# Kernel tuning notes

Measured on AMD Instinct MI355X. Metric: run time of the kernel, lower is better.

## Reference

```python
import jax, jax.numpy as jnp
import numpy as np

B, S, HID = 2, 2048, 2048
NH, NKV, HD = 16, 8, 128
GATE = NH  # headwise gate logits
KV_DIM = NKV * HD
QKV_OUT = NH * HD + GATE + 2 * KV_DIM  # 4112


def rotate_half(x):
    x1, x2 = jnp.split(x, 2, axis=-1)
    return jnp.concatenate([-x2, x1], axis=-1)


def setup_inputs() -> dict:
    key = jax.random.key(0)
    k1, k2, k3, k4, k5 = jax.random.split(key, 5)
    return {
        "hidden_states": jax.random.normal(k1, (B, S, HID), dtype=jnp.float32),
        "cos": jax.random.uniform(k2, (S, HD), dtype=jnp.float32),
        "sin": jax.random.uniform(k3, (S, HD), dtype=jnp.float32),
        "w_qkv": jax.random.normal(k4, (QKV_OUT, HID), dtype=jnp.float32) * (1.0 / HID ** 0.5),
        "w_o": jax.random.normal(k5, (HID, NH * HD), dtype=jnp.float32) * (1.0 / (NH * HD) ** 0.5),
    }


def reference(hidden_states, cos, sin, w_qkv, w_o):
    b, s, _ = hidden_states.shape
    qkv = hidden_states @ w_qkv.T  # [B,S,4112]
    q = qkv[..., :HID].reshape(b, s, NH, HD)
    gate = qkv[..., HID:HID + GATE]  # [B,S,NH]
    k = qkv[..., HID + GATE:HID + GATE + KV_DIM].reshape(b, s, NKV, HD)
    v = qkv[..., HID + GATE + KV_DIM:].reshape(b, s, NKV, HD)
    # RoPE (cos/sin broadcast over batch and heads)
    c = cos[None, :, None, :]
    sn = sin[None, :, None, :]
    q = q * c + rotate_half(q) * sn
    k = k * c + rotate_half(k) * sn
    # GQA: repeat kv heads (repeat_interleave on head axis)
    rep = NH // NKV
    k = jnp.repeat(k, rep, axis=2)
    v = jnp.repeat(v, rep, axis=2)
    scores = jnp.einsum("bqhd,bkhd->bhqk", q, k) / jnp.sqrt(jnp.float32(HD))
    attn = jax.nn.softmax(scores, axis=-1)
    out = jnp.einsum("bhqk,bkhd->bqhd", attn, v)  # [B,S,NH,HD]
    out = out * jax.nn.sigmoid(gate)[..., None]  # headwise gate
    out = out.reshape(b, s, NH * HD)
    return out @ w_o.T
```

## Files before the change

kernel.cpp:

```cpp
#include <hip/hip_runtime.h>
#include <math.h>

constexpr int cB   = 2;
constexpr int cS   = 2048;
constexpr int cHID = 2048;
constexpr int cNH  = 16;
constexpr int cNKV = 8;
constexpr int cHD  = 128;
constexpr int cQKV = 4112;
constexpr int cM   = cB * cS;
constexpr int cK   = 2048;

constexpr int cKO2 = 2048;
constexpr int cVO2 = 3072;
constexpr int cGO2 = 4096;

typedef short v8s __attribute__((ext_vector_type(8)));
typedef _Float16 v8h __attribute__((ext_vector_type(8)));
typedef float v4f __attribute__((ext_vector_type(4)));

static __device__ __forceinline__ unsigned short f2h(float f) {
    return __builtin_bit_cast(unsigned short, (_Float16)f);
}

#define GLD16(gp, lp)                                                          \
    __builtin_amdgcn_global_load_lds(                                          \
        (const __attribute__((address_space(1))) void*)(gp),                   \
        (__attribute__((address_space(3))) void*)(lp), 16, 0, 0)

template<int N> static __device__ __forceinline__ void vmwait() {
    asm volatile("s_waitcnt vmcnt(%0)" :: "n"(N) : "memory");
}
static __device__ __forceinline__ void lgkm0() {
    asm volatile("s_waitcnt lgkmcnt(0)" ::: "memory");
    __builtin_amdgcn_sched_barrier(0);
}
static __device__ __forceinline__ void barrier_() {
    __builtin_amdgcn_sched_barrier(0);
    __builtin_amdgcn_s_barrier();
    __builtin_amdgcn_sched_barrier(0);
}

__global__ __launch_bounds__(256) void split_math(const float* __restrict__ X,
                                                  unsigned short* __restrict__ H,
                                                  int rows)
{
    int idx = blockIdx.x * 256 + threadIdx.x;
    int c4 = idx & 511;
    int r  = idx >> 9;
    float4 v = make_float4(0.f, 0.f, 0.f, 0.f);
    if (r < rows) v = *(const float4*)&X[(size_t)r * cK + c4 * 4];
    *(ushort4*)&H[(size_t)r * cK + c4 * 4] =
        make_ushort4(f2h(v.x), f2h(v.y), f2h(v.z), f2h(v.w));
}

__global__ __launch_bounds__(256) void split_maqkv(const float* __restrict__ X,
                                                   unsigned short* __restrict__ H)
{
    int idx = blockIdx.x * 256 + threadIdx.x;
    int c4 = idx & 511;
    int r  = idx >> 9;
    int src = r + (r >= cHID ? 16 : 0);
    float4 v = *(const float4*)&X[(size_t)src * cK + c4 * 4];
    *(ushort4*)&H[(size_t)r * cK + c4 * 4] =
        make_ushort4(f2h(v.x), f2h(v.y), f2h(v.z), f2h(v.w));
}

template<int MF, int NF, bool TWOPASS>
__global__ __launch_bounds__(512, 2) void gemm8p(const unsigned short* __restrict__ Ah,
                                                 const unsigned short* __restrict__ Al,
                                                 const unsigned short* __restrict__ Bh,
                                                 float* __restrict__ C, int ldc,
                                                 float outScale, int nxt)
{
    constexpr int NWM = 16 / MF;
    constexpr int BN  = 16 * NF * (8 / NWM);
    constexpr int BSZ = BN * 32;
    constexpr int LB  = BN / 128;
    constexpr int L   = 2 + LB;
    constexpr int NT  = (TWOPASS ? 2 : 1) * (cK / 32);

    __shared__ __align__(16) unsigned short sA[4 * 8192];
    __shared__ __align__(16) unsigned short sB[4 * BSZ];

    const int tid = threadIdx.x;
    const int lane = tid & 63, w = tid >> 6;
    const int rl = lane & 15, quad = lane >> 4;
    const int wm = (w % NWM) * 16 * MF;
    const int wn = (w / NWM) * 16 * NF;

    const int nwg = gridDim.x;
    const int qx = nwg >> 3;
    const int wg = (blockIdx.x & 7) * qx + (blockIdx.x >> 3);
    const int bm = (wg / nxt) * 256;
    const int bn = (wg % nxt) * BN;

    const int srow = lane >> 2;
    const int gc = ((lane & 3) ^ ((lane >> 3) & 3)) * 8;
    const int fc = (quad ^ ((rl >> 1) & 3)) * 8;

    const size_t aOff = (size_t)(bm + 2 * w * 16 + srow) * cK + gc;
    const size_t bOff = (size_t)(bn + (LB == 2 ? 2 * w : w) * 16 + srow) * cK + gc;
    unsigned short* dA0 = sA + 2 * w * 512;
    unsigned short* dA1 = sA + (2 * w + 1) * 512;
    unsigned short* dB0 = sB + (LB == 2 ? 2 * w : w) * 512;
    unsigned short* dB1 = sB + ((LB == 2 ? 2 * w + 1 : 0)) * 512;

    v4f acc[MF][NF];
#pragma unroll
    for (int i = 0; i < MF; ++i)
#pragma unroll
        for (int j = 0; j < NF; ++j) acc[i][j] = (v4f){0.f, 0.f, 0.f, 0.f};

    auto stageA = [&](int t, int buf) {
        const unsigned short* pl = TWOPASS ? ((t & 1) ? Al : Ah) : Ah;
        const size_t ko = (size_t)(TWOPASS ? (t >> 1) : t) * 32;
        GLD16(pl + aOff + ko, dA0 + buf * 8192);
        GLD16(pl + aOff + 16 * cK + ko, dA1 + buf * 8192);
    };
    auto stageB = [&](int t, int buf) {
        const size_t ko = (size_t)(TWOPASS ? (t >> 1) : t) * 32;
        GLD16(Bh + bOff + ko, dB0 + buf * BSZ);
        if (LB == 2) GLD16(Bh + bOff + 16 * cK + ko, dB1 + buf * BSZ);
    };

    stageA(0, 0); stageB(0, 0);
    stageA(1, 1); stageB(1, 1);
    stageA(2, 2); stageB(2, 2);

    for (int t = 0; t < NT; ++t) {
        if (t < NT - 2)       vmwait<2 * L>();
        else if (t == NT - 2) vmwait<L>();
        else                  vmwait<0>();
        barrier_();

        const int cur = t & 3;
        const unsigned short* bufA = sA + cur * 8192;
        const unsigned short* bufB = sB + cur * BSZ;

        v8h af[MF], bf[NF / 2];
#pragma unroll
        for (int i = 0; i < MF; ++i)
            af[i] = *(const v8h*)&bufA[(wm + 16 * i + rl) * 32 + fc];
#pragma unroll
        for (int j = 0; j < NF / 2; ++j)
            bf[j] = *(const v8h*)&bufB[(wn + 16 * j + rl) * 32 + fc];
        if (t + 3 < NT) stageA(t + 3, (t + 3) & 3);
        lgkm0();
        __builtin_amdgcn_s_setprio(1);
#pragma unroll
        for (int i = 0; i < MF; ++i)
#pragma unroll
            for (int j = 0; j < NF / 2; ++j)
                acc[i][j] = __builtin_amdgcn_mfma_f32_16x16x32_f16(af[i], bf[j], acc[i][j], 0, 0, 0);
        __builtin_amdgcn_s_setprio(0);
        barrier_();

        v8h bg[NF / 2];
#pragma unroll
        for (int j = 0; j < NF / 2; ++j)
            bg[j] = *(const v8h*)&bufB[(wn + 16 * (NF / 2 + j) + rl) * 32 + fc];
        if (t + 3 < NT) stageB(t + 3, (t + 3) & 3);
        lgkm0();
        __builtin_amdgcn_s_setprio(1);
#pragma unroll
        for (int i = 0; i < MF; ++i)
#pragma unroll
            for (int j = 0; j < NF / 2; ++j)
                acc[i][NF / 2 + j] = __builtin_amdgcn_mfma_f32_16x16x32_f16(af[i], bg[j], acc[i][NF / 2 + j], 0, 0, 0);
        __builtin_amdgcn_s_setprio(0);
    }

#pragma unroll
    for (int i = 0; i < MF; ++i)
#pragma unroll
        for (int j = 0; j < NF; ++j) {
            const int col = bn + wn + 16 * j + rl;
            const int row0 = bm + wm + 16 * i + quad * 4;
#pragma unroll
            for (int r = 0; r < 4; ++r)
                C[(size_t)(row0 + r) * ldc + col] = acc[i][j][r] * outScale;
        }
}

__global__ __launch_bounds__(256) void gate_kernel(const float* __restrict__ hidden,
                                                   const float* __restrict__ w_qkv,
                                                   float* __restrict__ qkv)
{
    const int lane = threadIdx.x & 63, wv = threadIdx.x >> 6;
    const int m = blockIdx.x * 4 + wv;
    const float* hp = hidden + (size_t)m * cK;
    float4 h4[8];
#pragma unroll
    for (int i = 0; i < 8; ++i) h4[i] = *(const float4*)&hp[i * 256 + lane * 4];
#pragma unroll 1
    for (int g = 0; g < 16; ++g) {
        const float* wp = w_qkv + (size_t)(cHID + g) * cK;
        float acc = 0.f;
#pragma unroll
        for (int i = 0; i < 8; ++i) {
            float4 w4 = *(const float4*)&wp[i * 256 + lane * 4];
            acc = fmaf(h4[i].x, w4.x, acc);
            acc = fmaf(h4[i].y, w4.y, acc);
            acc = fmaf(h4[i].z, w4.z, acc);
            acc = fmaf(h4[i].w, w4.w, acc);
        }
#pragma unroll
        for (int k = 1; k < 64; k <<= 1) acc += __shfl_xor(acc, k);
        if (lane == 0) qkv[(size_t)m * cQKV + cGO2 + g] = acc;
    }
}

__global__ __launch_bounds__(256) void rope_q_kernel(float* __restrict__ qkv,
                                                     const float* __restrict__ cosp,
                                                     const float* __restrict__ sinp)
{
    int idx = blockIdx.x * 256 + threadIdx.x;
    int d = idx & 63;
    int t = idx >> 6;
    int head = t & (cNH - 1);
    int m = t >> 4;
    size_t base = (size_t)m * cQKV + head * cHD;
    int s = m & (cS - 1);
    float x1 = qkv[base + d], x2 = qkv[base + d + 64];
    float c1 = cosp[s * cHD + d], c2 = cosp[s * cHD + d + 64];
    float s1 = sinp[s * cHD + d], s2 = sinp[s * cHD + d + 64];
    qkv[base + d]      = x1 * c1 - x2 * s1;
    qkv[base + d + 64] = x2 * c2 + x1 * s2;
}

__global__ __launch_bounds__(256) void ropek_vt_kernel(const float* __restrict__ qkv,
                                                       const float* __restrict__ cosp,
                                                       const float* __restrict__ sinp,
                                                       unsigned short* __restrict__ Kh,
                                                       unsigned short* __restrict__ Vh)
{
    const int t = threadIdx.x;
    const int tile = blockIdx.x, kv = blockIdx.y, b = blockIdx.z;

#pragma unroll
    for (int i = 0; i < 8; ++i) {
        int e = i * 256 + t;
        int row = e >> 4;
        int c4 = e & 15;
        int s = tile * 128 + row;
        const float* kp = &qkv[(size_t)(b * cS + s) * cQKV + cKO2 + kv * cHD];
        float4 x1 = *(const float4*)&kp[c4 * 4];
        float4 x2 = *(const float4*)&kp[c4 * 4 + 64];
        float4 c1 = *(const float4*)&cosp[s * cHD + c4 * 4];
        float4 c2 = *(const float4*)&cosp[s * cHD + c4 * 4 + 64];
        float4 s1 = *(const float4*)&sinp[s * cHD + c4 * 4];
        float4 s2 = *(const float4*)&sinp[s * cHD + c4 * 4 + 64];
        ushort4 lo = make_ushort4(f2h(x1.x * c1.x - x2.x * s1.x),
                                  f2h(x1.y * c1.y - x2.y * s1.y),
                                  f2h(x1.z * c1.z - x2.z * s1.z),
                                  f2h(x1.w * c1.w - x2.w * s1.w));
        ushort4 hi = make_ushort4(f2h(x2.x * c2.x + x1.x * s2.x),
                                  f2h(x2.y * c2.y + x1.y * s2.y),
                                  f2h(x2.z * c2.z + x1.z * s2.z),
                                  f2h(x2.w * c2.w + x1.w * s2.w));
        size_t o = ((size_t)((b * cNKV + kv) * cS + s)) * cHD;
        *(ushort4*)&Kh[o + c4 * 4]      = lo;
        *(ushort4*)&Kh[o + c4 * 4 + 64] = hi;
    }

    __shared__ float T[128 * 132];
#pragma unroll
    for (int i = 0; i < 16; ++i) {
        int e = i * 256 + t;
        int row = e >> 5, c4 = e & 31;
        *(float4*)&T[row * 132 + c4 * 4] =
            *(const float4*)&qkv[(size_t)(b * cS + tile * 128 + row) * cQKV + cVO2 + kv * cHD + c4 * 4];
    }
    __syncthreads();
    const int d = t >> 1, half = t & 1;
    size_t ob = ((size_t)((b * cNKV + kv) * cHD + d)) * cS + tile * 128 + half * 64;
#pragma unroll
    for (int i = 0; i < 8; ++i) {
        unsigned short hh[8];
#pragma unroll
        for (int j = 0; j < 8; ++j)
            hh[j] = f2h(T[(half * 64 + i * 8 + j) * 132 + d]);
        *(ushort4*)&Vh[ob + i * 8]     = make_ushort4(hh[0], hh[1], hh[2], hh[3]);
        *(ushort4*)&Vh[ob + i * 8 + 4] = make_ushort4(hh[4], hh[5], hh[6], hh[7]);
    }
}

__global__ __launch_bounds__(512, 2) void attn_mfma(const float* __restrict__ qkv,
                                                    const unsigned short* __restrict__ Kh,
                                                    const unsigned short* __restrict__ Vh,
                                                    unsigned short* __restrict__ Oh)
{
    __shared__ __align__(16) char smem[65536];
    unsigned short* sKh = (unsigned short*)smem;
    unsigned short* sVh = (unsigned short*)(smem + 32768);

    const int tid = threadIdx.x;
    const int lane = tid & 63, w = tid >> 6;
    const int wh = w & 3, half = w >> 2;
    const int rl = lane & 15, quad = lane >> 4;
    const int qt = blockIdx.x, h = blockIdx.y, b = blockIdx.z;
    const int kvh = h >> 1;
    const float sc = 0.08838834764831845f * 1.4426950408889634f;

    v8h Qh[2][4];
#pragma unroll
    for (int mt = 0; mt < 2; ++mt) {
        const float* qp0 = &qkv[(size_t)(b * cS + qt * 128 + wh * 32 + mt * 16 + rl) * cQKV
                                + h * cHD + quad * 8];
#pragma unroll
        for (int c = 0; c < 4; ++c) {
            float4 x0 = *(const float4*)(qp0 + c * 32);
            float4 x1 = *(const float4*)(qp0 + c * 32 + 4);
            float f[8] = {x0.x, x0.y, x0.z, x0.w, x1.x, x1.y, x1.z, x1.w};
            v8s qh;
#pragma unroll
            for (int j = 0; j < 8; ++j) qh[j] = (short)f2h(f[j]);
            Qh[mt][c] = __builtin_bit_cast(v8h, qh);
        }
    }

    float l_i[2] = {0.f, 0.f};
    v4f O[2][8];
#pragma unroll
    for (int mt = 0; mt < 2; ++mt)
#pragma unroll
        for (int dt = 0; dt < 8; ++dt) O[mt][dt] = (v4f){0.f, 0.f, 0.f, 0.f};

    const size_t kbase = ((size_t)((b * cNKV + kvh) * cS)) * cHD;
    const size_t vbase = ((size_t)((b * cNKV + kvh) * cHD)) * cS;

    const int kchunk = 4 * wh + (lane >> 5);
    const int krow = lane & 31;
    const unsigned short* gKh0 = Kh + kbase + (size_t)krow * cHD + kchunk * 8;
    const unsigned short* gVh0 = Vh + vbase + (size_t)lane * cS + wh * 8;
    unsigned short* dKh0 = sKh + half * 8192 + wh * 1024;
    unsigned short* dVh0 = sVh + half * 8192 + wh * 1024;

#define STAGE(kt_, buf_)                                                         \
    do {                                                                         \
        const size_t ko_ = (size_t)(kt_) * (32 * cHD);                           \
        const size_t vo_ = (size_t)(kt_) * 32;                                   \
        const int bo_ = (buf_) * 4096;                                           \
        GLD16(gKh0 + ko_, dKh0 + bo_); GLD16(gKh0 + ko_ + 16, dKh0 + bo_ + 512); \
        GLD16(gVh0 + vo_, dVh0 + bo_);                                           \
        GLD16(gVh0 + vo_ + 64 * (size_t)cS, dVh0 + bo_ + 512);                   \
    } while (0)

    const int kt0 = half * 32;
    STAGE(kt0, 0);
    __syncthreads();

    for (int t = 0; t < 32; ++t) {
        const int cur = t & 1;
        const int cbo = half * 8192 + cur * 4096;

        v8h kf[4][2];
#pragma unroll
        for (int c = 0; c < 4; ++c)
#pragma unroll
            for (int nt = 0; nt < 2; ++nt)
                kf[c][nt] = *(const v8h*)&sKh[cbo + ((4 * c + quad) * 32 + nt * 16 + rl) * 8];

        if (t + 1 < 32) STAGE(kt0 + t + 1, cur ^ 1);

        v4f S[2][2];
#pragma unroll
        for (int mt = 0; mt < 2; ++mt)
#pragma unroll
            for (int nt = 0; nt < 2; ++nt) S[mt][nt] = (v4f){0.f, 0.f, 0.f, 0.f};
        __builtin_amdgcn_s_setprio(1);
#pragma unroll
        for (int c = 0; c < 4; ++c)
#pragma unroll
            for (int nt = 0; nt < 2; ++nt)
#pragma unroll
                for (int mt = 0; mt < 2; ++mt)
                    S[mt][nt] = __builtin_amdgcn_mfma_f32_16x16x32_f16(kf[c][nt], Qh[mt][c], S[mt][nt], 0, 0, 0);
        __builtin_amdgcn_s_setprio(0);

        v8h PhB[2];
#pragma unroll
        for (int mt = 0; mt < 2; ++mt) {
            float p[8];
#pragma unroll
            for (int nt = 0; nt < 2; ++nt)
#pragma unroll
                for (int r = 0; r < 4; ++r) {
                    float e = exp2f(fmaf(S[mt][nt][r], sc, -10.f));
                    p[nt * 4 + r] = e;
                    l_i[mt] += e;
                }
            int pk[4];
#pragma unroll
            for (int r = 0; r < 4; ++r)
                pk[r] = __builtin_bit_cast(int,
                        __builtin_amdgcn_cvt_pkrtz(p[4 + r], p[r]));
            const int q2 = (quad & 1) * 2;
            const int hiHalf = quad >> 1;
            v8s ph;
#pragma unroll
            for (int jj = 0; jj < 8; ++jj) {
                int srcl = (q2 + (jj >> 2)) * 16 + rl;
                int v = __shfl(pk[jj & 3], srcl);
                ph[jj] = hiHalf ? (short)(v & 0xffff) : (short)(((unsigned)v) >> 16);
            }
            PhB[mt] = __builtin_bit_cast(v8h, ph);
        }

        __builtin_amdgcn_s_setprio(1);
#pragma unroll
        for (int dt = 0; dt < 8; ++dt) {
            v8h vh = *(const v8h*)&sVh[cbo + (quad * 128 + dt * 16 + rl) * 8];
#pragma unroll
            for (int mt = 0; mt < 2; ++mt)
                O[mt][dt] = __builtin_amdgcn_mfma_f32_16x16x32_f16(vh, PhB[mt], O[mt][dt], 0, 0, 0);
        }
        __builtin_amdgcn_s_setprio(0);
        __syncthreads();
    }
#undef STAGE

    float* xO = (float*)smem;
    float* xL = (float*)(smem + 32768);
    if (half == 1) {
#pragma unroll
        for (int mt = 0; mt < 2; ++mt)
            xL[(mt * 4 + wh) * 64 + lane] = l_i[mt];
#pragma unroll
        for (int dt = 0; dt < 8; ++dt)
            *(v4f*)&xO[((wh * 8 + dt) * 64 + lane) * 4] = O[0][dt];
    }
    __syncthreads();
    if (half == 0) {
#pragma unroll
        for (int mt = 0; mt < 2; ++mt)
            l_i[mt] += xL[(mt * 4 + wh) * 64 + lane];
#pragma unroll
        for (int dt = 0; dt < 8; ++dt)
            O[0][dt] += *(const v4f*)&xO[((wh * 8 + dt) * 64 + lane) * 4];
    }
    __syncthreads();
    if (half == 1) {
#pragma unroll
        for (int dt = 0; dt < 8; ++dt)
            *(v4f*)&xO[((wh * 8 + dt) * 64 + lane) * 4] = O[1][dt];
    }
    __syncthreads();
    if (half == 0) {
#pragma unroll
        for (int dt = 0; dt < 8; ++dt)
            O[1][dt] += *(const v4f*)&xO[((wh * 8 + dt) * 64 + lane) * 4];

#pragma unroll
        for (int mt = 0; mt < 2; ++mt) {
            float lt = l_i[mt];
            lt += __shfl_xor(lt, 16);
            lt += __shfl_xor(lt, 32);
            int grow = b * cS + qt * 128 + wh * 32 + mt * 16 + rl;
            float g = qkv[(size_t)grow * cQKV + cGO2 + h];
            float u = 16.f / ((1.f + __expf(-g)) * lt);
            size_t obase = (size_t)grow * cHID + h * cHD + quad * 4;
#pragma unroll
            for (int dt = 0; dt < 8; ++dt) {
                *(ushort4*)&Oh[obase + dt * 16] =
                    make_ushort4(f2h(O[mt][dt][0] * u), f2h(O[mt][dt][1] * u),
                                 f2h(O[mt][dt][2] * u), f2h(O[mt][dt][3] * u));
            }
        }
    }
}

extern "C" void kernel_launch(void* const* d_in, const int* in_sizes, int n_in,
                              void* d_out, int out_size, void* d_ws, size_t ws_size,
                              hipStream_t stream)
{
    (void)in_sizes; (void)n_in; (void)out_size; (void)ws_size;
    const float* hidden = (const float*)d_in[0];
    const float* cosp   = (const float*)d_in[1];
    const float* sinp   = (const float*)d_in[2];
    const float* w_qkv  = (const float*)d_in[3];
    const float* w_o    = (const float*)d_in[4];
    float* out = (float*)d_out;

    char* ws = (char*)d_ws;
    float* qkv = (float*)ws;
    unsigned short* Bh = (unsigned short*)(ws + 67371008);
    unsigned short* Kh = (unsigned short*)(ws + 101974016);
    const size_t kvPlane = (size_t)cB * cNKV * cS * cHD;
    unsigned short* Vh = Kh + kvPlane;

    unsigned short* Ahid = (unsigned short*)d_out;
    unsigned short* Oh = Bh;
    unsigned short* Wh = Kh;

    split_math<<<dim3(cM * (cK / 4) / 256), 256, 0, stream>>>(hidden, Ahid, cM);
    split_maqkv<<<dim3(4096 * (cK / 4) / 256), 256, 0, stream>>>(w_qkv, Bh);

    gemm8p<8, 4, false><<<dim3(256), 512, 0, stream>>>(Ahid, Ahid, Bh, qkv, cQKV, 1.0f, 16);

    gate_kernel<<<dim3(cM / 4), 256, 0, stream>>>(hidden, w_qkv, qkv);

    rope_q_kernel<<<dim3(cM * cNH * (cHD / 2) / 256), 256, 0, stream>>>(qkv, cosp, sinp);

    ropek_vt_kernel<<<dim3(cS / 128, cNKV, cB), 256, 0, stream>>>(qkv, cosp, sinp, Kh, Vh);

    attn_mfma<<<dim3(cS / 128, cNH, cB), 512, 0, stream>>>(qkv, Kh, Vh, Oh);

    split_math<<<dim3(cHID * (cK / 4) / 256), 256, 0, stream>>>(w_o, Wh, cHID);

    gemm8p<4, 4, false><<<dim3(256), 512, 0, stream>>>(Oh, Oh, Wh, out, cHID, 1.0f / 16.0f, 16);
}
```

Baseline: 404.2 us.

## Emit fp16 Q/K/V directly from QKV GEMM epilogue and fuse Q RoPE into attention

The QKV GEMM epilogue now writes Q, K and V as fp16 in attention-ready layouts (V transposed) instead of an fp32 qkv buffer. The separate rope_q and ropek_vt kernels are replaced by a small K-only RoPE kernel, and Q RoPE is applied inside the attention kernel on load. Gate logits go to a compact buffer. This removes the fp32 round trips through global memory and two launches. In exchange the GEMM epilogue does scattered stores, and K is rounded to fp16 before RoPE is applied.

```diff
diff --git a/kernel.cpp b/kernel.cpp
--- a/kernel.cpp
+++ b/kernel.cpp
@@ -11,16 +11,15 @@
 constexpr int cM   = cB * cS;
 constexpr int cK   = 2048;
 
-constexpr int cKO2 = 2048;
-constexpr int cVO2 = 3072;
-constexpr int cGO2 = 4096;
-
 typedef short v8s __attribute__((ext_vector_type(8)));
 typedef _Float16 v8h __attribute__((ext_vector_type(8)));
 typedef float v4f __attribute__((ext_vector_type(4)));
 
 static __device__ __forceinline__ unsigned short f2h(float f) {
     return __builtin_bit_cast(unsigned short, (_Float16)f);
+}
+static __device__ __forceinline__ float h2f(unsigned short u) {
+    return (float)__builtin_bit_cast(_Float16, u);
 }
 
 #define GLD16(gp, lp)                                                          \
@@ -66,19 +65,21 @@
         make_ushort4(f2h(v.x), f2h(v.y), f2h(v.z), f2h(v.w));
 }
 
-template<int MF, int NF, bool TWOPASS>
+template<int MF, int NF, bool QKVOUT>
 __global__ __launch_bounds__(512, 2) void gemm8p(const unsigned short* __restrict__ Ah,
-                                                 const unsigned short* __restrict__ Al,
                                                  const unsigned short* __restrict__ Bh,
                                                  float* __restrict__ C, int ldc,
-                                                 float outScale, int nxt)
+                                                 float outScale, int nxt,
+                                                 unsigned short* __restrict__ Q16,
+                                                 unsigned short* __restrict__ K16,
+                                                 unsigned short* __restrict__ V16)
 {
     constexpr int NWM = 16 / MF;
     constexpr int BN  = 16 * NF * (8 / NWM);
     constexpr int BSZ = BN * 32;
     constexpr int LB  = BN / 128;
     constexpr int L   = 2 + LB;
-    constexpr int NT  = (TWOPASS ? 2 : 1) * (cK / 32);
+    constexpr int NT  = cK / 32;
 
     __shared__ __align__(16) unsigned short sA[4 * 8192];
     __shared__ __align__(16) unsigned short sB[4 * BSZ];
@@ -113,13 +114,12 @@
         for (int j = 0; j < NF; ++j) acc[i][j] = (v4f){0.f, 0.f, 0.f, 0.f};
 
     auto stageA = [&](int t, int buf) {
-        const unsigned short* pl = TWOPASS ? ((t & 1) ? Al : Ah) : Ah;
-        const size_t ko = (size_t)(TWOPASS ? (t >> 1) : t) * 32;
-        GLD16(pl + aOff + ko, dA0 + buf * 8192);
-        GLD16(pl + aOff + 16 * cK + ko, dA1 + buf * 8192);
+        const size_t ko = (size_t)t * 32;
+        GLD16(Ah + aOff + ko, dA0 + buf * 8192);
+        GLD16(Ah + aOff + 16 * cK + ko, dA1 + buf * 8192);
     };
     auto stageB = [&](int t, int buf) {
-        const size_t ko = (size_t)(TWOPASS ? (t >> 1) : t) * 32;
+        const size_t ko = (size_t)t * 32;
         GLD16(Bh + bOff + ko, dB0 + buf * BSZ);
         if (LB == 2) GLD16(Bh + bOff + 16 * cK + ko, dB1 + buf * BSZ);
     };
@@ -175,17 +175,40 @@
     for (int i = 0; i < MF; ++i)
 #pragma unroll
         for (int j = 0; j < NF; ++j) {
-            const int col = bn + wn + 16 * j + rl;
+            const int colg = bn + wn + 16 * j;
+            const int col  = colg + rl;
             const int row0 = bm + wm + 16 * i + quad * 4;
-#pragma unroll
-            for (int r = 0; r < 4; ++r)
-                C[(size_t)(row0 + r) * ldc + col] = acc[i][j][r] * outScale;
+            if (!QKVOUT) {
+#pragma unroll
+                for (int r = 0; r < 4; ++r)
+                    C[(size_t)(row0 + r) * ldc + col] = acc[i][j][r] * outScale;
+            } else {
+                if (colg < 2048) {
+#pragma unroll
+                    for (int r = 0; r < 4; ++r)
+                        Q16[(size_t)(row0 + r) * cHID + col] = f2h(acc[i][j][r]);
+                } else if (colg < 3072) {
+                    const int cc = col - 2048, kv = cc >> 7, d = cc & 127;
+#pragma unroll
+                    for (int r = 0; r < 4; ++r) {
+                        const int row = row0 + r;
+                        K16[((size_t)((row >> 11) * cNKV + kv) * cS + (row & 2047)) * cHD + d] =
+                            f2h(acc[i][j][r]);
+                    }
+                } else {
+                    const int cc = col - 3072, kv = cc >> 7, d = cc & 127;
+                    const int b_ = row0 >> 11, s0 = row0 & 2047;
+                    *(ushort4*)&V16[((size_t)(b_ * cNKV + kv) * cHD + d) * cS + s0] =
+                        make_ushort4(f2h(acc[i][j][0]), f2h(acc[i][j][1]),
+                                     f2h(acc[i][j][2]), f2h(acc[i][j][3]));
+                }
+            }
         }
 }
 
 __global__ __launch_bounds__(256) void gate_kernel(const float* __restrict__ hidden,
                                                    const float* __restrict__ w_qkv,
-                                                   float* __restrict__ qkv)
+                                                   float* __restrict__ gateBuf)
 {
     const int lane = threadIdx.x & 63, wv = threadIdx.x >> 6;
     const int m = blockIdx.x * 4 + wv;
@@ -207,86 +230,41 @@
         }
 #pragma unroll
         for (int k = 1; k < 64; k <<= 1) acc += __shfl_xor(acc, k);
-        if (lane == 0) qkv[(size_t)m * cQKV + cGO2 + g] = acc;
-    }
-}
-
-__global__ __launch_bounds__(256) void rope_q_kernel(float* __restrict__ qkv,
-                                                     const float* __restrict__ cosp,
-                                                     const float* __restrict__ sinp)
+        if (lane == 0) gateBuf[(size_t)m * 16 + g] = acc;
+    }
+}
+
+__global__ __launch_bounds__(256) void ropek_kernel(const unsigned short* __restrict__ Kpre,
+                                                    const float* __restrict__ cosp,
+                                                    const float* __restrict__ sinp,
+                                                    unsigned short* __restrict__ Kh)
 {
     int idx = blockIdx.x * 256 + threadIdx.x;
-    int d = idx & 63;
-    int t = idx >> 6;
-    int head = t & (cNH - 1);
-    int m = t >> 4;
-    size_t base = (size_t)m * cQKV + head * cHD;
-    int s = m & (cS - 1);
-    float x1 = qkv[base + d], x2 = qkv[base + d + 64];
-    float c1 = cosp[s * cHD + d], c2 = cosp[s * cHD + d + 64];
-    float s1 = sinp[s * cHD + d], s2 = sinp[s * cHD + d + 64];
-    qkv[base + d]      = x1 * c1 - x2 * s1;
-    qkv[base + d + 64] = x2 * c2 + x1 * s2;
-}
-
-__global__ __launch_bounds__(256) void ropek_vt_kernel(const float* __restrict__ qkv,
-                                                       const float* __restrict__ cosp,
-                                                       const float* __restrict__ sinp,
-                                                       unsigned short* __restrict__ Kh,
-                                                       unsigned short* __restrict__ Vh)
-{
-    const int t = threadIdx.x;
-    const int tile = blockIdx.x, kv = blockIdx.y, b = blockIdx.z;
-
-#pragma unroll
-    for (int i = 0; i < 8; ++i) {
-        int e = i * 256 + t;
-        int row = e >> 4;
-        int c4 = e & 15;
-        int s = tile * 128 + row;
-        const float* kp = &qkv[(size_t)(b * cS + s) * cQKV + cKO2 + kv * cHD];
-        float4 x1 = *(const float4*)&kp[c4 * 4];
-        float4 x2 = *(const float4*)&kp[c4 * 4 + 64];
-        float4 c1 = *(const float4*)&cosp[s * cHD + c4 * 4];
-        float4 c2 = *(const float4*)&cosp[s * cHD + c4 * 4 + 64];
-        float4 s1 = *(const float4*)&sinp[s * cHD + c4 * 4];
-        float4 s2 = *(const float4*)&sinp[s * cHD + c4 * 4 + 64];
-        ushort4 lo = make_ushort4(f2h(x1.x * c1.x - x2.x * s1.x),
-                                  f2h(x1.y * c1.y - x2.y * s1.y),
-                                  f2h(x1.z * c1.z - x2.z * s1.z),
-                                  f2h(x1.w * c1.w - x2.w * s1.w));
-        ushort4 hi = make_ushort4(f2h(x2.x * c2.x + x1.x * s2.x),
-                                  f2h(x2.y * c2.y + x1.y * s2.y),
-                                  f2h(x2.z * c2.z + x1.z * s2.z),
-                                  f2h(x2.w * c2.w + x1.w * s2.w));
-        size_t o = ((size_t)((b * cNKV + kv) * cS + s)) * cHD;
-        *(ushort4*)&Kh[o + c4 * 4]      = lo;
-        *(ushort4*)&Kh[o + c4 * 4 + 64] = hi;
-    }
-
-    __shared__ float T[128 * 132];
-#pragma unroll
-    for (int i = 0; i < 16; ++i) {
-        int e = i * 256 + t;
-        int row = e >> 5, c4 = e & 31;
-        *(float4*)&T[row * 132 + c4 * 4] =
-            *(const float4*)&qkv[(size_t)(b * cS + tile * 128 + row) * cQKV + cVO2 + kv * cHD + c4 * 4];
-    }
-    __syncthreads();
-    const int d = t >> 1, half = t & 1;
-    size_t ob = ((size_t)((b * cNKV + kv) * cHD + d)) * cS + tile * 128 + half * 64;
-#pragma unroll
-    for (int i = 0; i < 8; ++i) {
-        unsigned short hh[8];
-#pragma unroll
-        for (int j = 0; j < 8; ++j)
-            hh[j] = f2h(T[(half * 64 + i * 8 + j) * 132 + d]);
-        *(ushort4*)&Vh[ob + i * 8]     = make_ushort4(hh[0], hh[1], hh[2], hh[3]);
-        *(ushort4*)&Vh[ob + i * 8 + 4] = make_ushort4(hh[4], hh[5], hh[6], hh[7]);
-    }
-}
-
-__global__ __launch_bounds__(512, 2) void attn_mfma(const float* __restrict__ qkv,
+    int d4 = idx & 15;
+    int s  = (idx >> 4) & 2047;
+    int kv = (idx >> 15) & 7;
+    int b  = idx >> 18;
+    size_t base = ((size_t)((b * cNKV + kv) * cS) + s) * cHD;
+    ushort4 x1u = *(const ushort4*)&Kpre[base + d4 * 4];
+    ushort4 x2u = *(const ushort4*)&Kpre[base + d4 * 4 + 64];
+    float4 c1 = *(const float4*)&cosp[s * cHD + d4 * 4];
+    float4 c2 = *(const float4*)&cosp[s * cHD + d4 * 4 + 64];
+    float4 s1 = *(const float4*)&sinp[s * cHD + d4 * 4];
+    float4 s2 = *(const float4*)&sinp[s * cHD + d4 * 4 + 64];
+    float x1x = h2f(x1u.x), x1y = h2f(x1u.y), x1z = h2f(x1u.z), x1w = h2f(x1u.w);
+    float x2x = h2f(x2u.x), x2y = h2f(x2u.y), x2z = h2f(x2u.z), x2w = h2f(x2u.w);
+    *(ushort4*)&Kh[base + d4 * 4] =
+        make_ushort4(f2h(x1x * c1.x - x2x * s1.x), f2h(x1y * c1.y - x2y * s1.y),
+                     f2h(x1z * c1.z - x2z * s1.z), f2h(x1w * c1.w - x2w * s1.w));
+    *(ushort4*)&Kh[base + d4 * 4 + 64] =
+        make_ushort4(f2h(x2x * c2.x + x1x * s2.x), f2h(x2y * c2.y + x1y * s2.y),
+                     f2h(x2z * c2.z + x1z * s2.z), f2h(x2w * c2.w + x1w * s2.w));
+}
+
+__global__ __launch_bounds__(512, 2) void attn_mfma(const unsigned short* __restrict__ Q16,
+                                                    const float* __restrict__ gateBuf,
+                                                    const float* __restrict__ cosp,
+                                                    const float* __restrict__ sinp,
                                                     const unsigned short* __restrict__ Kh,
                                                     const unsigned short* __restrict__ Vh,
                                                     unsigned short* __restrict__ Oh)
@@ -306,17 +284,40 @@
     v8h Qh[2][4];
 #pragma unroll
     for (int mt = 0; mt < 2; ++mt) {
-        const float* qp0 = &qkv[(size_t)(b * cS + qt * 128 + wh * 32 + mt * 16 + rl) * cQKV
-                                + h * cHD + quad * 8];
+        const int sq = qt * 128 + wh * 32 + mt * 16 + rl;
+        const unsigned short* qp0 = &Q16[(size_t)(b * cS + sq) * cHID + h * cHD + quad * 8];
+        float f[4][8];
 #pragma unroll
         for (int c = 0; c < 4; ++c) {
-            float4 x0 = *(const float4*)(qp0 + c * 32);
-            float4 x1 = *(const float4*)(qp0 + c * 32 + 4);
-            float f[8] = {x0.x, x0.y, x0.z, x0.w, x1.x, x1.y, x1.z, x1.w};
-            v8s qh;
-#pragma unroll
-            for (int j = 0; j < 8; ++j) qh[j] = (short)f2h(f[j]);
-            Qh[mt][c] = __builtin_bit_cast(v8h, qh);
+            v8h qv = *(const v8h*)(qp0 + c * 32);
+#pragma unroll
+            for (int jj = 0; jj < 8; ++jj) f[c][jj] = (float)qv[jj];
+        }
+        const float* cp = &cosp[sq * cHD + quad * 8];
+        const float* sp = &sinp[sq * cHD + quad * 8];
+#pragma unroll
+        for (int c = 0; c < 2; ++c) {
+            float4 c1a = *(const float4*)(cp + c * 32);
+            float4 c1b = *(const float4*)(cp + c * 32 + 4);
+            float4 c2a = *(const float4*)(cp + c * 32 + 64);
+            float4 c2b = *(const float4*)(cp + c * 32 + 68);
+            float4 s1a = *(const float4*)(sp + c * 32);
+            float4 s1b = *(const float4*)(sp + c * 32 + 4);
+            float4 s2a = *(const float4*)(sp + c * 32 + 64);
+            float4 s2b = *(const float4*)(sp + c * 32 + 68);
+            float C1[8] = {c1a.x, c1a.y, c1a.z, c1a.w, c1b.x, c1b.y, c1b.z, c1b.w};
+            float C2[8] = {c2a.x, c2a.y, c2a.z, c2a.w, c2b.x, c2b.y, c2b.z, c2b.w};
+            float S1[8] = {s1a.x, s1a.y, s1a.z, s1a.w, s1b.x, s1b.y, s1b.z, s1b.w};
+            float S2[8] = {s2a.x, s2a.y, s2a.z, s2a.w, s2b.x, s2b.y, s2b.z, s2b.w};
+            v8s q1, q2;
+#pragma unroll
+            for (int jj = 0; jj < 8; ++jj) {
+                float x1 = f[c][jj], x2 = f[c + 2][jj];
+                q1[jj] = (short)f2h(x1 * C1[jj] - x2 * S1[jj]);
+                q2[jj] = (short)f2h(x2 * C2[jj] + x1 * S2[jj]);
+            }
+            Qh[mt][c]     = __builtin_bit_cast(v8h, q1);
+            Qh[mt][c + 2] = __builtin_bit_cast(v8h, q2);
         }
     }
 
@@ -458,7 +459,7 @@
             lt += __shfl_xor(lt, 16);
             lt += __shfl_xor(lt, 32);
             int grow = b * cS + qt * 128 + wh * 32 + mt * 16 + rl;
-            float g = qkv[(size_t)grow * cQKV + cGO2 + h];
+            float g = gateBuf[(size_t)grow * 16 + h];
             float u = 16.f / ((1.f + __expf(-g)) * lt);
             size_t obase = (size_t)grow * cHID + h * cHD + quad * 4;
 #pragma unroll
@@ -484,30 +485,32 @@
     float* out = (float*)d_out;
 
     char* ws = (char*)d_ws;
-    float* qkv = (float*)ws;
-    unsigned short* Bh = (unsigned short*)(ws + 67371008);
-    unsigned short* Kh = (unsigned short*)(ws + 101974016);
-    const size_t kvPlane = (size_t)cB * cNKV * cS * cHD;
-    unsigned short* Vh = Kh + kvPlane;
+    unsigned short* Q16  = (unsigned short*)ws;
+    unsigned short* Bh   = (unsigned short*)(ws + 16777216);
+    unsigned short* Kpre = (unsigned short*)(ws + 33554432);
+    unsigned short* Kh   = (unsigned short*)(ws + 41943040);
+    unsigned short* Vh   = (unsigned short*)(ws + 50331648);
+    float*          gateBuf = (float*)(ws + 58720256);
 
     unsigned short* Ahid = (unsigned short*)d_out;
     unsigned short* Oh = Bh;
-    unsigned short* Wh = Kh;
+    unsigned short* Wh = Kpre;
 
     split_math<<<dim3(cM * (cK / 4) / 256), 256, 0, stream>>>(hidden, Ahid, cM);
     split_maqkv<<<dim3(4096 * (cK / 4) / 256), 256, 0, stream>>>(w_qkv, Bh);
 
-    gemm8p<8, 4, false><<<dim3(256), 512, 0, stream>>>(Ahid, Ahid, Bh, qkv, cQKV, 1.0f, 16);
-
-    gate_kernel<<<dim3(cM / 4), 256, 0, stream>>>(hidden, w_qkv, qkv);
-
-    rope_q_kernel<<<dim3(cM * cNH * (cHD / 2) / 256), 256, 0, stream>>>(qkv, cosp, sinp);
-
-    ropek_vt_kernel<<<dim3(cS / 128, cNKV, cB), 256, 0, stream>>>(qkv, cosp, sinp, Kh, Vh);
-
-    attn_mfma<<<dim3(cS / 128, cNH, cB), 512, 0, stream>>>(qkv, Kh, Vh, Oh);
+    gemm8p<8, 4, true><<<dim3(256), 512, 0, stream>>>(
+        Ahid, Bh, nullptr, 0, 1.0f, 16, Q16, Kpre, Vh);
+
+    gate_kernel<<<dim3(cM / 4), 256, 0, stream>>>(hidden, w_qkv, gateBuf);
+
+    ropek_kernel<<<dim3(2048), 256, 0, stream>>>(Kpre, cosp, sinp, Kh);
+
+    attn_mfma<<<dim3(cS / 128, cNH, cB), 512, 0, stream>>>(
+        Q16, gateBuf, cosp, sinp, Kh, Vh, Oh);
 
     split_math<<<dim3(cHID * (cK / 4) / 256), 256, 0, stream>>>(w_o, Wh, cHID);
 
-    gemm8p<4, 4, false><<<dim3(256), 512, 0, stream>>>(Oh, Oh, Wh, out, cHID, 1.0f / 16.0f, 16);
-}
+    gemm8p<4, 4, false><<<dim3(256), 512, 0, stream>>>(
+        Oh, Wh, out, cHID, 1.0f / 16.0f, 16, nullptr, nullptr, nullptr);
+}
```

Result: faster. 388.4 us (-3.9%).
